# Performance work log

Measured on AMD Instinct MI355X. Metric: run time of the kernel, lower is better.

## Reference

```python
import jax, jax.numpy as jnp
import numpy as np

NUM_HEADS = 16
NEG_BIG = 1e9


def setup_inputs() -> dict:
    key = jax.random.key(0)
    k1, k2, k3 = jax.random.split(key, 3)
    B, T, D = 2, 2048, 1024
    x = jax.random.normal(k1, (B, T, D), dtype=jnp.float32)
    W_attn = jax.random.normal(k2, (D, 3 * D), dtype=jnp.float32) * 0.02
    b_attn = jnp.zeros((3 * D,), dtype=jnp.float32)
    W_proj = jax.random.normal(k3, (D, D), dtype=jnp.float32) * 0.02
    b_proj = jnp.zeros((D,), dtype=jnp.float32)
    return {"x": x, "W_attn": W_attn, "b_attn": b_attn, "W_proj": W_proj, "b_proj": b_proj}


def reference(x, W_attn, b_attn, W_proj, b_proj):
    B, T, D = x.shape
    H = NUM_HEADS
    dh = D // H
    # qkv projection (GPT-style Conv1D == linear)
    qkv = jnp.einsum('btd,de->bte', x, W_attn) + b_attn  # [B,T,3D]
    q, k, v = jnp.split(qkv, 3, axis=-1)
    # split heads -> [B,H,T,dh]
    q = q.reshape(B, T, H, dh).transpose(0, 2, 1, 3)
    k = k.reshape(B, T, H, dh).transpose(0, 2, 1, 3)
    v = v.reshape(B, T, H, dh).transpose(0, 2, 1, 3)
    # scores [B,H,T,T]; scale=True divides by sqrt(head_dim)
    w = jnp.einsum('bhqd,bhkd->bhqk', q, k) / jnp.sqrt(jnp.float32(dh))
    # causal mask: multiplicative tril then large additive negative, as in source
    mask = jnp.tril(jnp.ones((T, T), dtype=w.dtype))[None, None, :, :]
    w = w * mask - NEG_BIG * (1.0 - mask)
    p = jax.nn.softmax(w, axis=-1)  # attn dropout = identity (eval mode)
    out = jnp.einsum('bhqk,bhkd->bhqd', p, v)  # [B,H,T,dh]
    out = out.transpose(0, 2, 1, 3).reshape(B, T, D)  # merge heads
    out = jnp.einsum('btd,de->bte', out, W_proj) + b_proj  # residual dropout = identity
    return out
```

## Files before the change

kernel.cpp:

```cpp
#include <hip/hip_runtime.h>

typedef unsigned short u16;
typedef unsigned u32;
typedef __bf16 bf16x8 __attribute__((ext_vector_type(8)));
typedef __bf16 bf16x2 __attribute__((ext_vector_type(2)));
typedef float f32x4 __attribute__((ext_vector_type(4)));
typedef u16 u16x4 __attribute__((ext_vector_type(4)));
typedef u32 u32x2 __attribute__((ext_vector_type(2)));
typedef u32 u32x4 __attribute__((ext_vector_type(4)));

__device__ __forceinline__ u16 f2bf(float f) {
  u32 u = __float_as_uint(f);
  u += 0x7fffu + ((u >> 16) & 1u);
  return (u16)(u >> 16);
}

__device__ __forceinline__ u32 pk2(float a, float b) {
#if __has_builtin(__builtin_amdgcn_cvt_pk_bf16_f32)
  bf16x2 r = __builtin_amdgcn_cvt_pk_bf16_f32(a, b);
  return __builtin_bit_cast(u32, r);
#else
  return (u32)f2bf(a) | ((u32)f2bf(b) << 16);
#endif
}

__device__ __forceinline__ float fast_exp2(float x) {
  return __builtin_amdgcn_exp2f(x);
}

__device__ __forceinline__ void gload16(const u16* g, u16* l) {
  __builtin_amdgcn_global_load_lds((__attribute__((address_space(1))) void*)g,
                                   (__attribute__((address_space(3))) void*)l,
                                   16, 0, 0);
}

__global__ __launch_bounds__(256) void cvt_f32_bf16(const float* __restrict__ in,
                                                    u16* __restrict__ out, int n4) {
  int i = blockIdx.x * 256 + threadIdx.x;
  if (i >= n4) return;
  float4 v = ((const float4*)in)[i];
  u16x4 o = { f2bf(v.x), f2bf(v.y), f2bf(v.z), f2bf(v.w) };
  ((u16x4*)out)[i] = o;
}

__global__ __launch_bounds__(256) void transpose_cvt(const float* __restrict__ in,
                                                     u16* __restrict__ out, int R, int C) {
  __shared__ float tile[32][33];
  int c0 = blockIdx.x * 32, r0 = blockIdx.y * 32;
  int tx = threadIdx.x & 31, ty = threadIdx.x >> 5;
#pragma unroll
  for (int i = 0; i < 32; i += 8)
    tile[ty + i][tx] = in[(size_t)(r0 + ty + i) * C + c0 + tx];
  __syncthreads();
#pragma unroll
  for (int i = 0; i < 32; i += 8)
    out[(size_t)(c0 + ty + i) * R + r0 + tx] = f2bf(tile[tx][ty + i]);
}

template <int EPI>
__global__ __launch_bounds__(256) void gemm_bt(const u16* __restrict__ A,
                                               const u16* __restrict__ Bt, int K,
                                               const float* __restrict__ bias,
                                               float* __restrict__ outF,
                                               u16* __restrict__ qb, u16* __restrict__ kb,
                                               u16* __restrict__ vtb) {
  __shared__ __align__(16) u16 As[128 * 32];
  __shared__ __align__(16) u16 Bs[128 * 32];
  const int tid = threadIdx.x;
  const int w = tid >> 6, lane = tid & 63, quad = lane >> 4, l16 = lane & 15;
  const int wm = w >> 1, wn = w & 1;
  const int tm = blockIdx.y * 128, tn = blockIdx.x * 128;

  f32x4 acc[4][4] = {};

  const int ra = lane >> 2;
  const int ca = (lane & 3) * 8;
  const u16* gA0 = A + (size_t)(tm + w * 16 + ra) * K + ca;
  const u16* gA1 = A + (size_t)(tm + (w + 4) * 16 + ra) * K + ca;
  const u16* gB0 = Bt + (size_t)(tn + w * 16 + ra) * K + ca;
  const u16* gB1 = Bt + (size_t)(tn + (w + 4) * 16 + ra) * K + ca;
  u16* lA0 = &As[(w * 16) * 32];
  u16* lA1 = &As[((w + 4) * 16) * 32];
  u16* lB0 = &Bs[(w * 16) * 32];
  u16* lB1 = &Bs[((w + 4) * 16) * 32];

  for (int k0 = 0; k0 < K; k0 += 32) {
    gload16(gA0 + k0, lA0);
    gload16(gA1 + k0, lA1);
    gload16(gB0 + k0, lB0);
    gload16(gB1 + k0, lB1);
    __syncthreads();
    bf16x8 af[4], bfr[4];
#pragma unroll
    for (int mt = 0; mt < 4; ++mt)
      af[mt] = *(const bf16x8*)&As[(wm * 64 + mt * 16 + l16) * 32 + quad * 8];
#pragma unroll
    for (int nt = 0; nt < 4; ++nt)
      bfr[nt] = *(const bf16x8*)&Bs[(wn * 64 + nt * 16 + l16) * 32 + quad * 8];
#pragma unroll
    for (int mt = 0; mt < 4; ++mt)
#pragma unroll
      for (int nt = 0; nt < 4; ++nt)
        acc[mt][nt] = __builtin_amdgcn_mfma_f32_16x16x32_bf16(af[mt], bfr[nt], acc[mt][nt], 0, 0, 0);
    __syncthreads();
  }

#pragma unroll
  for (int mt = 0; mt < 4; ++mt) {
#pragma unroll
    for (int nt = 0; nt < 4; ++nt) {
      const int row0 = tm + wm * 64 + mt * 16 + quad * 4;
      const int col = tn + wn * 64 + nt * 16 + l16;
      float v4[4];
#pragma unroll
      for (int r = 0; r < 4; ++r) v4[r] = acc[mt][nt][r] + bias[col];
      if (EPI == 0) {
        int which = col >> 10, d = col & 1023, hh = d >> 6, dd = d & 63;
        int b = row0 >> 11, t = row0 & 2047;
        int bh = (b << 4) + hh;
        if (which == 0) {
#pragma unroll
          for (int r = 0; r < 4; ++r)
            qb[((size_t)bh * 2048 + t + r) * 64 + dd] = f2bf(v4[r] * 0.18033688f);
        } else if (which == 1) {
#pragma unroll
          for (int r = 0; r < 4; ++r)
            kb[((size_t)bh * 2048 + t + r) * 64 + dd] = f2bf(v4[r]);
        } else {
          u16x4 pk = { f2bf(v4[0]), f2bf(v4[1]), f2bf(v4[2]), f2bf(v4[3]) };
          *(u16x4*)(vtb + ((size_t)bh * 64 + dd) * 2048 + t) = pk;
        }
      } else {
#pragma unroll
        for (int r = 0; r < 4; ++r)
          outF[(size_t)(row0 + r) * 1024 + col] = v4[r];
      }
    }
  }
}

__global__ __launch_bounds__(256) void flash_attn(const u16* __restrict__ qb,
                                                  const u16* __restrict__ kb,
                                                  const u16* __restrict__ vtb,
                                                  u16* __restrict__ ao) {
  const int T = 2048;
  const int tid = threadIdx.x;
  const int w = tid >> 6, lane = tid & 63;
  const int quad = lane >> 4, l16 = lane & 15;
  const int bx = blockIdx.x;
  const int bh = bx >> 5;
  const int g0 = bx & 31;
  const int G = ((bh >> 3) & 1) ? (31 - g0) : g0;
  const int b = bh >> 4, h = bh & 15;
  const int qrow = G * 64 + w * 16 + l16;
  const size_t kvbase = (size_t)bh * T * 64;
  const int nkt = G + 1;

  __shared__ __align__(16) u16 Ks[64][72];
  __shared__ __align__(16) u16 Vs[64][72];
  __shared__ __align__(16) u16 Ps[4][16][72];

  bf16x8 q0 = *(const bf16x8*)(qb + kvbase + (size_t)qrow * 64 + quad * 8);
  bf16x8 q1 = *(const bf16x8*)(qb + kvbase + (size_t)qrow * 64 + 32 + quad * 8);

  float lp = 0.f;
  f32x4 o[4] = {};

  const int tok = tid >> 2, c4 = (tid & 3) * 16;
  const u16* kg = kb + kvbase + (size_t)tok * 64 + c4;
  const u16* vg = vtb + (size_t)(bh * 64 + tok) * 2048 + c4;

  {
    u32x4 a0 = *(const u32x4*)(kg);
    u32x4 a1 = *(const u32x4*)(kg + 8);
    u32x4 b0 = *(const u32x4*)(vg);
    u32x4 b1 = *(const u32x4*)(vg + 8);
    *(u32x4*)&Ks[tok][c4] = a0;  *(u32x4*)&Ks[tok][c4 + 8] = a1;
    *(u32x4*)&Vs[tok][c4] = b0;  *(u32x4*)&Vs[tok][c4 + 8] = b1;
  }
  __syncthreads();

  u32x4 sk0, sk1, sv0, sv1;

  for (int kt = 0; kt < nkt; ++kt) {
    const bool more = (kt + 1 < nkt);
    if (more) {
      const int kb2 = (kt + 1) * 64;
      sk0 = *(const u32x4*)(kg + (size_t)kb2 * 64);
      sk1 = *(const u32x4*)(kg + (size_t)kb2 * 64 + 8);
      sv0 = *(const u32x4*)(vg + kb2);
      sv1 = *(const u32x4*)(vg + kb2 + 8);
    }

    f32x4 z[4];
#pragma unroll
    for (int st = 0; st < 4; ++st) {
      bf16x8 kf0 = *(const bf16x8*)&Ks[st * 16 + l16][quad * 8];
      bf16x8 kf1 = *(const bf16x8*)&Ks[st * 16 + l16][32 + quad * 8];
      f32x4 zz = {};
      zz = __builtin_amdgcn_mfma_f32_16x16x32_bf16(kf0, q0, zz, 0, 0, 0);
      zz = __builtin_amdgcn_mfma_f32_16x16x32_bf16(kf1, q1, zz, 0, 0, 0);
      z[st] = zz;
    }
    if (kt == nkt - 1) {
      const int ro = w * 16 + l16;
#pragma unroll
      for (int st = 0; st < 4; ++st)
#pragma unroll
        for (int r = 0; r < 4; ++r)
          if (st * 16 + quad * 4 + r > ro) z[st][r] = -1e30f;
    }
#pragma unroll
    for (int st = 0; st < 4; ++st) {
      float p0 = fast_exp2(z[st][0]), p1 = fast_exp2(z[st][1]);
      float p2 = fast_exp2(z[st][2]), p3 = fast_exp2(z[st][3]);
      lp += (p0 + p1) + (p2 + p3);
      u32x2 pw = { pk2(p0, p1), pk2(p2, p3) };
      *(u32x2*)&Ps[w][l16][st * 16 + quad * 4] = pw;
    }
    __asm__ __volatile__("s_waitcnt lgkmcnt(0)" ::: "memory");

    bf16x8 pf0 = *(const bf16x8*)&Ps[w][l16][quad * 8];
    bf16x8 pf1 = *(const bf16x8*)&Ps[w][l16][32 + quad * 8];
#pragma unroll
    for (int dt = 0; dt < 4; ++dt) {
      bf16x8 vf0 = *(const bf16x8*)&Vs[dt * 16 + l16][quad * 8];
      bf16x8 vf1 = *(const bf16x8*)&Vs[dt * 16 + l16][32 + quad * 8];
      o[dt] = __builtin_amdgcn_mfma_f32_16x16x32_bf16(vf0, pf0, o[dt], 0, 0, 0);
      o[dt] = __builtin_amdgcn_mfma_f32_16x16x32_bf16(vf1, pf1, o[dt], 0, 0, 0);
    }

    __syncthreads();
    if (more) {
      *(u32x4*)&Ks[tok][c4] = sk0;  *(u32x4*)&Ks[tok][c4 + 8] = sk1;
      *(u32x4*)&Vs[tok][c4] = sv0;  *(u32x4*)&Vs[tok][c4 + 8] = sv1;
    }
    __syncthreads();
  }

  lp += __shfl_xor(lp, 16);
  lp += __shfl_xor(lp, 32);
  float inv = 1.0f / lp;
  size_t obase = ((size_t)b * T + qrow) * 1024 + h * 64;
#pragma unroll
  for (int dt = 0; dt < 4; ++dt) {
    u16x4 ov = { f2bf(o[dt][0] * inv), f2bf(o[dt][1] * inv),
                 f2bf(o[dt][2] * inv), f2bf(o[dt][3] * inv) };
    *(u16x4*)(ao + obase + dt * 16 + quad * 4) = ov;
  }
}

extern "C" void kernel_launch(void* const* d_in, const int* in_sizes, int n_in,
                              void* d_out, int out_size, void* d_ws, size_t ws_size,
                              hipStream_t stream) {
  const float* x      = (const float*)d_in[0];
  const float* W_attn = (const float*)d_in[1];
  const float* b_attn = (const float*)d_in[2];
  const float* W_proj = (const float*)d_in[3];
  const float* b_proj = (const float*)d_in[4];
  float* out = (float*)d_out;

  if (ws_size < 50331648u) return;

  char* ws = (char*)d_ws;
  u16* xb  = (u16*)(ws);
  u16* wat = (u16*)(ws + 8388608u);
  u16* wpt = (u16*)(ws + 14680064u);
  u16* qb  = (u16*)(ws + 16777216u);
  u16* kb  = (u16*)(ws + 25165824u);
  u16* vtb = (u16*)(ws + 33554432u);
  u16* ao  = (u16*)(ws + 41943040u);

  cvt_f32_bf16<<<4096, 256, 0, stream>>>(x, xb, 4194304 / 4);
  transpose_cvt<<<dim3(96, 32), 256, 0, stream>>>(W_attn, wat, 1024, 3072);
  transpose_cvt<<<dim3(32, 32), 256, 0, stream>>>(W_proj, wpt, 1024, 1024);

  gemm_bt<0><<<dim3(24, 32), 256, 0, stream>>>(xb, wat, 1024, b_attn, nullptr, qb, kb, vtb);

  flash_attn<<<dim3(1024), 256, 0, stream>>>(qb, kb, vtb, ao);

  gemm_bt<1><<<dim3(8, 32), 256, 0, stream>>>(ao, wpt, 1024, b_proj, out, nullptr, nullptr, nullptr);
}
```

Baseline: 195.4 us.

## Split QKV GEMM into Q/K and V kernels with transposed MFMA stores

The QKV projection is split into two launches. One computes Q and K with swapped MFMA operands, so each lane holds 4 consecutive channels and writes packed 4-element bf16 stores. The other computes V and keeps the transposed V store. Flash attention now interleaves heads across consecutive blocks with a different causal-length ordering, and its LDS row padding shrinks from 72 to 68. This targets scattered 2-byte epilogue stores and aims for better load balance and cache locality, at the cost of an extra kernel launch and possible LDS bank conflicts from the new padding.

```diff
diff --git a/kernel.cpp b/kernel.cpp
--- a/kernel.cpp
+++ b/kernel.cpp
@@ -57,7 +57,7 @@
     out[(size_t)(c0 + ty + i) * R + r0 + tx] = f2bf(tile[tx][ty + i]);
 }
 
-template <int EPI>
+template <int MODE>
 __global__ __launch_bounds__(256) void gemm_bt(const u16* __restrict__ A,
                                                const u16* __restrict__ Bt, int K,
                                                const float* __restrict__ bias,
@@ -100,40 +100,57 @@
 #pragma unroll
     for (int mt = 0; mt < 4; ++mt)
 #pragma unroll
-      for (int nt = 0; nt < 4; ++nt)
-        acc[mt][nt] = __builtin_amdgcn_mfma_f32_16x16x32_bf16(af[mt], bfr[nt], acc[mt][nt], 0, 0, 0);
+      for (int nt = 0; nt < 4; ++nt) {
+        if (MODE == 0)
+          acc[mt][nt] = __builtin_amdgcn_mfma_f32_16x16x32_bf16(bfr[nt], af[mt], acc[mt][nt], 0, 0, 0);
+        else
+          acc[mt][nt] = __builtin_amdgcn_mfma_f32_16x16x32_bf16(af[mt], bfr[nt], acc[mt][nt], 0, 0, 0);
+      }
     __syncthreads();
   }
 
-#pragma unroll
-  for (int mt = 0; mt < 4; ++mt) {
-#pragma unroll
-    for (int nt = 0; nt < 4; ++nt) {
-      const int row0 = tm + wm * 64 + mt * 16 + quad * 4;
-      const int col = tn + wn * 64 + nt * 16 + l16;
-      float v4[4];
-#pragma unroll
-      for (int r = 0; r < 4; ++r) v4[r] = acc[mt][nt][r] + bias[col];
-      if (EPI == 0) {
-        int which = col >> 10, d = col & 1023, hh = d >> 6, dd = d & 63;
-        int b = row0 >> 11, t = row0 & 2047;
-        int bh = (b << 4) + hh;
-        if (which == 0) {
-#pragma unroll
-          for (int r = 0; r < 4; ++r)
-            qb[((size_t)bh * 2048 + t + r) * 64 + dd] = f2bf(v4[r] * 0.18033688f);
-        } else if (which == 1) {
-#pragma unroll
-          for (int r = 0; r < 4; ++r)
-            kb[((size_t)bh * 2048 + t + r) * 64 + dd] = f2bf(v4[r]);
-        } else {
+  if (MODE == 0) {
+    const int which = tn >> 10;
+    u16* dst = which ? kb : qb;
+    const float scale = which ? 1.0f : 0.18033688f;
+#pragma unroll
+    for (int mt = 0; mt < 4; ++mt) {
+#pragma unroll
+      for (int nt = 0; nt < 4; ++nt) {
+        const int t = tm + wm * 64 + mt * 16 + l16;
+        const int ch = tn + wn * 64 + nt * 16 + quad * 4;
+        const int d = ch & 1023, hh = d >> 6, dd = d & 63;
+        const int b = t >> 11, tt = t & 2047;
+        const int bh = (b << 4) + hh;
+        float4 b4 = *(const float4*)&bias[ch];
+        u16x4 pk = { f2bf((acc[mt][nt][0] + b4.x) * scale),
+                     f2bf((acc[mt][nt][1] + b4.y) * scale),
+                     f2bf((acc[mt][nt][2] + b4.z) * scale),
+                     f2bf((acc[mt][nt][3] + b4.w) * scale) };
+        *(u16x4*)(dst + ((size_t)bh * 2048 + tt) * 64 + dd) = pk;
+      }
+    }
+  } else {
+#pragma unroll
+    for (int mt = 0; mt < 4; ++mt) {
+#pragma unroll
+      for (int nt = 0; nt < 4; ++nt) {
+        const int row0 = tm + wm * 64 + mt * 16 + quad * 4;
+        const int col = tn + wn * 64 + nt * 16 + l16;
+        float v4[4];
+#pragma unroll
+        for (int r = 0; r < 4; ++r) v4[r] = acc[mt][nt][r] + bias[col];
+        if (MODE == 1) {
+          const int hh = col >> 6, dd = col & 63;
+          const int b = row0 >> 11, t = row0 & 2047;
+          const int bh = (b << 4) + hh;
           u16x4 pk = { f2bf(v4[0]), f2bf(v4[1]), f2bf(v4[2]), f2bf(v4[3]) };
           *(u16x4*)(vtb + ((size_t)bh * 64 + dd) * 2048 + t) = pk;
+        } else {
+#pragma unroll
+          for (int r = 0; r < 4; ++r)
+            outF[(size_t)(row0 + r) * 1024 + col] = v4[r];
         }
-      } else {
-#pragma unroll
-        for (int r = 0; r < 4; ++r)
-          outF[(size_t)(row0 + r) * 1024 + col] = v4[r];
       }
     }
   }
@@ -148,17 +165,17 @@
   const int w = tid >> 6, lane = tid & 63;
   const int quad = lane >> 4, l16 = lane & 15;
   const int bx = blockIdx.x;
-  const int bh = bx >> 5;
-  const int g0 = bx & 31;
-  const int G = ((bh >> 3) & 1) ? (31 - g0) : g0;
+  const int bh = bx & 31;
+  const int g0 = bx >> 5;
+  const int G = ((g0 >> 3) & 1) ? ((g0 & 24) | (7 - (g0 & 7))) : g0;
   const int b = bh >> 4, h = bh & 15;
   const int qrow = G * 64 + w * 16 + l16;
   const size_t kvbase = (size_t)bh * T * 64;
   const int nkt = G + 1;
 
-  __shared__ __align__(16) u16 Ks[64][72];
-  __shared__ __align__(16) u16 Vs[64][72];
-  __shared__ __align__(16) u16 Ps[4][16][72];
+  __shared__ __align__(16) u16 Ks[64][68];
+  __shared__ __align__(16) u16 Vs[64][68];
+  __shared__ __align__(16) u16 Ps[4][16][68];
 
   bf16x8 q0 = *(const bf16x8*)(qb + kvbase + (size_t)qrow * 64 + quad * 8);
   bf16x8 q1 = *(const bf16x8*)(qb + kvbase + (size_t)qrow * 64 + 32 + quad * 8);
@@ -275,9 +292,11 @@
   transpose_cvt<<<dim3(96, 32), 256, 0, stream>>>(W_attn, wat, 1024, 3072);
   transpose_cvt<<<dim3(32, 32), 256, 0, stream>>>(W_proj, wpt, 1024, 1024);
 
-  gemm_bt<0><<<dim3(24, 32), 256, 0, stream>>>(xb, wat, 1024, b_attn, nullptr, qb, kb, vtb);
+  gemm_bt<0><<<dim3(16, 32), 256, 0, stream>>>(xb, wat, 1024, b_attn, nullptr, qb, kb, nullptr);
+  gemm_bt<1><<<dim3(8, 32), 256, 0, stream>>>(xb, wat + 2048 * 1024, 1024, b_attn + 2048,
+                                              nullptr, nullptr, nullptr, vtb);
 
   flash_attn<<<dim3(1024), 256, 0, stream>>>(qb, kb, vtb, ao);
 
-  gemm_bt<1><<<dim3(8, 32), 256, 0, stream>>>(ao, wpt, 1024, b_proj, out, nullptr, nullptr, nullptr);
-}
+  gemm_bt<2><<<dim3(8, 32), 256, 0, stream>>>(ao, wpt, 1024, b_proj, out, nullptr, nullptr, nullptr);
+}
```

Result: slower. 219.8 us (+12.5%).

## Pair causal query tiles G and 31-G per block to balance work and reuse K/V

Applied to the files above, without the earlier changes.

Each attention block now handles two query tiles, a short one (G) and its mirror (31-G), so every block does the same total causal work and the K/V tiles loaded into shared memory are reused by both tiles during the overlapping prefix. The grid halves from 1024 to 512 blocks. The aim is to remove load imbalance from causal tiles and cut redundant K/V loads. The cost is fewer blocks, which can lower occupancy and latency hiding, plus more registers for the two accumulator sets.

```diff
diff --git a/kernel.cpp b/kernel.cpp
--- a/kernel.cpp
+++ b/kernel.cpp
@@ -147,24 +147,26 @@
   const int tid = threadIdx.x;
   const int w = tid >> 6, lane = tid & 63;
   const int quad = lane >> 4, l16 = lane & 15;
-  const int bx = blockIdx.x;
-  const int bh = bx >> 5;
-  const int g0 = bx & 31;
-  const int G = ((bh >> 3) & 1) ? (31 - g0) : g0;
+  const int bh = blockIdx.x;
+  const int G = blockIdx.y;
   const int b = bh >> 4, h = bh & 15;
-  const int qrow = G * 64 + w * 16 + l16;
+  const int ro = w * 16 + l16;
+  const int rowA = G * 64 + ro;
+  const int rowB = (31 - G) * 64 + ro;
   const size_t kvbase = (size_t)bh * T * 64;
-  const int nkt = G + 1;
+  const int nkt = 32 - G;
 
   __shared__ __align__(16) u16 Ks[64][72];
   __shared__ __align__(16) u16 Vs[64][72];
-  __shared__ __align__(16) u16 Ps[4][16][72];
-
-  bf16x8 q0 = *(const bf16x8*)(qb + kvbase + (size_t)qrow * 64 + quad * 8);
-  bf16x8 q1 = *(const bf16x8*)(qb + kvbase + (size_t)qrow * 64 + 32 + quad * 8);
-
-  float lp = 0.f;
-  f32x4 o[4] = {};
+  __shared__ __align__(16) u16 Ps[4][2][16][72];
+
+  bf16x8 qA0 = *(const bf16x8*)(qb + kvbase + (size_t)rowA * 64 + quad * 8);
+  bf16x8 qA1 = *(const bf16x8*)(qb + kvbase + (size_t)rowA * 64 + 32 + quad * 8);
+  bf16x8 qB0 = *(const bf16x8*)(qb + kvbase + (size_t)rowB * 64 + quad * 8);
+  bf16x8 qB1 = *(const bf16x8*)(qb + kvbase + (size_t)rowB * 64 + 32 + quad * 8);
+
+  float lpA = 0.f, lpB = 0.f;
+  f32x4 oA[4] = {}, oB[4] = {};
 
   const int tok = tid >> 2, c4 = (tid & 3) * 16;
   const u16* kg = kb + kvbase + (size_t)tok * 64 + c4;
@@ -184,6 +186,7 @@
 
   for (int kt = 0; kt < nkt; ++kt) {
     const bool more = (kt + 1 < nkt);
+    const bool dual = (kt <= G);
     if (more) {
       const int kb2 = (kt + 1) * 64;
       sk0 = *(const u32x4*)(kg + (size_t)kb2 * 64);
@@ -192,42 +195,73 @@
       sv1 = *(const u32x4*)(vg + kb2 + 8);
     }
 
-    f32x4 z[4];
+    f32x4 zA[4], zB[4];
 #pragma unroll
     for (int st = 0; st < 4; ++st) {
       bf16x8 kf0 = *(const bf16x8*)&Ks[st * 16 + l16][quad * 8];
       bf16x8 kf1 = *(const bf16x8*)&Ks[st * 16 + l16][32 + quad * 8];
       f32x4 zz = {};
-      zz = __builtin_amdgcn_mfma_f32_16x16x32_bf16(kf0, q0, zz, 0, 0, 0);
-      zz = __builtin_amdgcn_mfma_f32_16x16x32_bf16(kf1, q1, zz, 0, 0, 0);
-      z[st] = zz;
+      zz = __builtin_amdgcn_mfma_f32_16x16x32_bf16(kf0, qB0, zz, 0, 0, 0);
+      zz = __builtin_amdgcn_mfma_f32_16x16x32_bf16(kf1, qB1, zz, 0, 0, 0);
+      zB[st] = zz;
+      if (dual) {
+        f32x4 za = {};
+        za = __builtin_amdgcn_mfma_f32_16x16x32_bf16(kf0, qA0, za, 0, 0, 0);
+        za = __builtin_amdgcn_mfma_f32_16x16x32_bf16(kf1, qA1, za, 0, 0, 0);
+        zA[st] = za;
+      }
     }
     if (kt == nkt - 1) {
-      const int ro = w * 16 + l16;
 #pragma unroll
       for (int st = 0; st < 4; ++st)
 #pragma unroll
         for (int r = 0; r < 4; ++r)
-          if (st * 16 + quad * 4 + r > ro) z[st][r] = -1e30f;
+          if (st * 16 + quad * 4 + r > ro) zB[st][r] = -1e30f;
+    }
+    if (dual && kt == G) {
+#pragma unroll
+      for (int st = 0; st < 4; ++st)
+#pragma unroll
+        for (int r = 0; r < 4; ++r)
+          if (st * 16 + quad * 4 + r > ro) zA[st][r] = -1e30f;
     }
 #pragma unroll
     for (int st = 0; st < 4; ++st) {
-      float p0 = fast_exp2(z[st][0]), p1 = fast_exp2(z[st][1]);
-      float p2 = fast_exp2(z[st][2]), p3 = fast_exp2(z[st][3]);
-      lp += (p0 + p1) + (p2 + p3);
+      float p0 = fast_exp2(zB[st][0]), p1 = fast_exp2(zB[st][1]);
+      float p2 = fast_exp2(zB[st][2]), p3 = fast_exp2(zB[st][3]);
+      lpB += (p0 + p1) + (p2 + p3);
       u32x2 pw = { pk2(p0, p1), pk2(p2, p3) };
-      *(u32x2*)&Ps[w][l16][st * 16 + quad * 4] = pw;
+      *(u32x2*)&Ps[w][1][l16][st * 16 + quad * 4] = pw;
+    }
+    if (dual) {
+#pragma unroll
+      for (int st = 0; st < 4; ++st) {
+        float p0 = fast_exp2(zA[st][0]), p1 = fast_exp2(zA[st][1]);
+        float p2 = fast_exp2(zA[st][2]), p3 = fast_exp2(zA[st][3]);
+        lpA += (p0 + p1) + (p2 + p3);
+        u32x2 pw = { pk2(p0, p1), pk2(p2, p3) };
+        *(u32x2*)&Ps[w][0][l16][st * 16 + quad * 4] = pw;
+      }
     }
     __asm__ __volatile__("s_waitcnt lgkmcnt(0)" ::: "memory");
 
-    bf16x8 pf0 = *(const bf16x8*)&Ps[w][l16][quad * 8];
-    bf16x8 pf1 = *(const bf16x8*)&Ps[w][l16][32 + quad * 8];
+    bf16x8 pfB0 = *(const bf16x8*)&Ps[w][1][l16][quad * 8];
+    bf16x8 pfB1 = *(const bf16x8*)&Ps[w][1][l16][32 + quad * 8];
+    bf16x8 pfA0, pfA1;
+    if (dual) {
+      pfA0 = *(const bf16x8*)&Ps[w][0][l16][quad * 8];
+      pfA1 = *(const bf16x8*)&Ps[w][0][l16][32 + quad * 8];
+    }
 #pragma unroll
     for (int dt = 0; dt < 4; ++dt) {
       bf16x8 vf0 = *(const bf16x8*)&Vs[dt * 16 + l16][quad * 8];
       bf16x8 vf1 = *(const bf16x8*)&Vs[dt * 16 + l16][32 + quad * 8];
-      o[dt] = __builtin_amdgcn_mfma_f32_16x16x32_bf16(vf0, pf0, o[dt], 0, 0, 0);
-      o[dt] = __builtin_amdgcn_mfma_f32_16x16x32_bf16(vf1, pf1, o[dt], 0, 0, 0);
+      oB[dt] = __builtin_amdgcn_mfma_f32_16x16x32_bf16(vf0, pfB0, oB[dt], 0, 0, 0);
+      oB[dt] = __builtin_amdgcn_mfma_f32_16x16x32_bf16(vf1, pfB1, oB[dt], 0, 0, 0);
+      if (dual) {
+        oA[dt] = __builtin_amdgcn_mfma_f32_16x16x32_bf16(vf0, pfA0, oA[dt], 0, 0, 0);
+        oA[dt] = __builtin_amdgcn_mfma_f32_16x16x32_bf16(vf1, pfA1, oA[dt], 0, 0, 0);
+      }
     }
 
     __syncthreads();
@@ -238,15 +272,27 @@
     __syncthreads();
   }
 
-  lp += __shfl_xor(lp, 16);
-  lp += __shfl_xor(lp, 32);
-  float inv = 1.0f / lp;
-  size_t obase = ((size_t)b * T + qrow) * 1024 + h * 64;
-#pragma unroll
-  for (int dt = 0; dt < 4; ++dt) {
-    u16x4 ov = { f2bf(o[dt][0] * inv), f2bf(o[dt][1] * inv),
-                 f2bf(o[dt][2] * inv), f2bf(o[dt][3] * inv) };
-    *(u16x4*)(ao + obase + dt * 16 + quad * 4) = ov;
+  lpA += __shfl_xor(lpA, 16); lpA += __shfl_xor(lpA, 32);
+  lpB += __shfl_xor(lpB, 16); lpB += __shfl_xor(lpB, 32);
+  {
+    float inv = 1.0f / lpA;
+    size_t obase = ((size_t)b * T + rowA) * 1024 + h * 64;
+#pragma unroll
+    for (int dt = 0; dt < 4; ++dt) {
+      u16x4 ov = { f2bf(oA[dt][0] * inv), f2bf(oA[dt][1] * inv),
+                   f2bf(oA[dt][2] * inv), f2bf(oA[dt][3] * inv) };
+      *(u16x4*)(ao + obase + dt * 16 + quad * 4) = ov;
+    }
+  }
+  {
+    float inv = 1.0f / lpB;
+    size_t obase = ((size_t)b * T + rowB) * 1024 + h * 64;
+#pragma unroll
+    for (int dt = 0; dt < 4; ++dt) {
+      u16x4 ov = { f2bf(oB[dt][0] * inv), f2bf(oB[dt][1] * inv),
+                   f2bf(oB[dt][2] * inv), f2bf(oB[dt][3] * inv) };
+      *(u16x4*)(ao + obase + dt * 16 + quad * 4) = ov;
+    }
   }
 }
 
@@ -277,7 +323,7 @@
 
   gemm_bt<0><<<dim3(24, 32), 256, 0, stream>>>(xb, wat, 1024, b_attn, nullptr, qb, kb, vtb);
 
-  flash_attn<<<dim3(1024), 256, 0, stream>>>(qb, kb, vtb, ao);
+  flash_attn<<<dim3(32, 16), 256, 0, stream>>>(qb, kb, vtb, ao);
 
   gemm_bt<1><<<dim3(8, 32), 256, 0, stream>>>(ao, wpt, 1024, b_proj, out, nullptr, nullptr, nullptr);
 }
```

Result: slower. 200.0 us (+2.4%).
